# Optimization experiments

Measured on AMD Instinct MI355X. Metric: run time of the kernel, lower is better.

## Reference

```python
import jax, jax.numpy as jnp
import numpy as np


def setup_inputs() -> dict:
    key0 = jax.random.key(0)
    kq, kk, kv, km = jax.random.split(key0, 4)
    B, H, S, Dk = 2, 16, 2048, 64
    query = jax.random.normal(kq, (B, H, S, Dk), dtype=jnp.float32)
    key = jax.random.normal(kk, (B, H, S, Dk), dtype=jnp.float32)
    value = jax.random.normal(kv, (B, H, S, Dk), dtype=jnp.float32)
    mask = jax.random.randint(km, (B, 1, 1, S), 0, 2, dtype=jnp.int32)
    return {"query": query, "key": key, "value": value, "mask": mask}


def reference(query, key, value, mask):
    d_k = query.shape[-1]
    scale = 1.0 / jnp.sqrt(jnp.asarray(d_k, dtype=query.dtype))
    # scores: [B, H, Sq, Sk]
    scores = jnp.einsum("bhqd,bhkd->bhqk", query, key) * scale
    scores = jnp.where(mask == 0, jnp.asarray(-1e9, dtype=scores.dtype), scores)
    attention_weights = jax.nn.softmax(scores, axis=-1)
    output = jnp.einsum("bhqk,bhkd->bhqd", attention_weights, value)
    return output, attention_weights
```

## Files before the change

### kernel.cpp

```cpp
#include <hip/hip_runtime.h>
#include <stdint.h>

#define S_LEN 2048
#define DK 64
#define MT 64
#define NT 64
#define LDP 72

typedef __attribute__((ext_vector_type(8))) short bf16x8;
typedef __attribute__((ext_vector_type(4))) float floatx4;

__device__ inline unsigned short f2bf(float f) {
    union { float f; unsigned u; } v; v.f = f;
    unsigned r = v.u + 0x7FFFu + ((v.u >> 16) & 1u);
    return (unsigned short)(r >> 16);
}

__device__ inline void async16(const void* g, void* l) {
    using gu32 = const __attribute__((address_space(1))) unsigned int;
    using lu32 = __attribute__((address_space(3))) unsigned int;
    gu32* gp = reinterpret_cast<gu32*>(reinterpret_cast<uintptr_t>(g));
    lu32* lp = reinterpret_cast<lu32*>(static_cast<unsigned int>(reinterpret_cast<uintptr_t>(l)));
    __builtin_amdgcn_global_load_lds(gp, lp, 16, 0, 0);
}

__global__ __launch_bounds__(256) void convert_qk(
    const float* __restrict__ Q, const float* __restrict__ K,
    unsigned short* __restrict__ Qb, unsigned short* __restrict__ Kb)
{
    int i = blockIdx.x * 256 + threadIdx.x;
    const int NQ = (2 * 16 * 2048 * 64) / 4;
    const float* src; unsigned short* dst; int j; float sc;
    if (i < NQ) { src = Q; dst = Qb; j = i; sc = 0.125f; }
    else        { src = K; dst = Kb; j = i - NQ; sc = 1.0f; }
    float4 f = ((const float4*)src)[j];
    ushort4 o;
    o.x = f2bf(f.x * sc); o.y = f2bf(f.y * sc);
    o.z = f2bf(f.z * sc); o.w = f2bf(f.w * sc);
    ((ushort4*)dst)[j] = o;
}

__global__ __launch_bounds__(256) void transpose_v(
    const float* __restrict__ V, unsigned short* __restrict__ Vt)
{
    __shared__ unsigned short t[64][72];
    const int head = blockIdx.y, kt = blockIdx.x, tid = threadIdx.x;
    const float* src = V + ((size_t)head * S_LEN + kt * 64) * DK;
    {
        const int r = tid >> 2, c = (tid & 3) * 16;
        #pragma unroll
        for (int i = 0; i < 4; ++i) {
            float4 f = *(const float4*)(src + r * DK + c + i * 4);
            t[r][c + i * 4 + 0] = f2bf(f.x);
            t[r][c + i * 4 + 1] = f2bf(f.y);
            t[r][c + i * 4 + 2] = f2bf(f.z);
            t[r][c + i * 4 + 3] = f2bf(f.w);
        }
    }
    __syncthreads();
    {
        const int d = tid >> 2, kb = (tid & 3) * 16;
        unsigned short tmp[16];
        #pragma unroll
        for (int j = 0; j < 16; ++j) tmp[j] = t[kb + j][d];
        unsigned short* dst = Vt + (size_t)head * DK * S_LEN + (size_t)d * S_LEN + kt * 64 + kb;
        ((uint4*)dst)[0] = *(const uint4*)&tmp[0];
        ((uint4*)dst)[1] = *(const uint4*)&tmp[8];
    }
}

__global__ __launch_bounds__(256) void sdpa_main(
    const unsigned short* __restrict__ Qb, const unsigned short* __restrict__ Kb,
    const unsigned short* __restrict__ Vt, const int* __restrict__ mask,
    float* __restrict__ O, float* __restrict__ W)
{
    __shared__ alignas(16) unsigned short qs[MT * DK];
    __shared__ alignas(16) unsigned short ks[NT * DK];
    __shared__ alignas(16) unsigned short vs[DK * NT];
    __shared__ alignas(16) unsigned short ps[MT * LDP];

    const int tid  = threadIdx.x;
    const int wave = tid >> 6;
    const int lane = tid & 63;
    const int quad = lane >> 4;
    const int l16  = lane & 15;

    const int head = blockIdx.y;
    const int bidx = head >> 4;
    const int q0   = blockIdx.x * MT;

    const unsigned short* Qh = Qb + ((size_t)head * S_LEN + q0) * DK;
    const unsigned short* Kh = Kb + (size_t)head * S_LEN * DK;
    const unsigned short* Vh = Vt + (size_t)head * DK * S_LEN;
    const int*   mk = mask + bidx * S_LEN;
    float* Wh = W + (size_t)head * S_LEN * S_LEN;
    float* Oh = O + (size_t)head * S_LEN * DK;

    {
        const int o0 = wave * 2048 + lane * 16;
        async16((const char*)Qh + o0,        (char*)qs + o0);
        async16((const char*)Qh + o0 + 1024, (char*)qs + o0 + 1024);
    }
    __syncthreads();
    const bf16x8 qa0 = *(const bf16x8*)&qs[(wave * 16 + l16) * DK + quad * 8];
    const bf16x8 qa1 = *(const bf16x8*)&qs[(wave * 16 + l16) * DK + 32 + quad * 8];

    float lsum[4] = {0.f, 0.f, 0.f, 0.f};
    for (int kt = 0; kt < S_LEN / NT; ++kt) {
        {
            const char* gb = (const char*)Kh + kt * 8192;
            const int o0 = wave * 2048 + lane * 16;
            async16(gb + o0,        (char*)ks + o0);
            async16(gb + o0 + 1024, (char*)ks + o0 + 1024);
        }
        float mf[4];
        #pragma unroll
        for (int c = 0; c < 4; ++c)
            mf[c] = mk[kt * NT + c * 16 + l16] ? 1.0f : 0.0f;
        __syncthreads();
        #pragma unroll
        for (int c = 0; c < 4; ++c) {
            bf16x8 b0 = *(const bf16x8*)&ks[(c * 16 + l16) * DK + quad * 8];
            bf16x8 b1 = *(const bf16x8*)&ks[(c * 16 + l16) * DK + 32 + quad * 8];
            floatx4 z = {0.f, 0.f, 0.f, 0.f};
            z = __builtin_amdgcn_mfma_f32_16x16x32_bf16(qa0, b0, z, 0, 0, 0);
            z = __builtin_amdgcn_mfma_f32_16x16x32_bf16(qa1, b1, z, 0, 0, 0);
            #pragma unroll
            for (int r = 0; r < 4; ++r)
                lsum[r] += __expf(z[r]) * mf[c];
        }
        __syncthreads();
    }
    float rl[4];
    #pragma unroll
    for (int r = 0; r < 4; ++r) {
        float s = lsum[r];
        #pragma unroll
        for (int off = 1; off < 16; off <<= 1)
            s += __shfl_xor(s, off, 64);
        rl[r] = 1.0f / s;
    }

    floatx4 oacc[4];
    #pragma unroll
    for (int c = 0; c < 4; ++c) oacc[c] = (floatx4){0.f, 0.f, 0.f, 0.f};

    for (int kt = 0; kt < S_LEN / NT; ++kt) {
        {
            const char* gb = (const char*)Kh + kt * 8192;
            const int o0 = wave * 2048 + lane * 16;
            async16(gb + o0,        (char*)ks + o0);
            async16(gb + o0 + 1024, (char*)ks + o0 + 1024);
        }
        {
            const int o0 = wave * 2048 + lane * 16;
            #pragma unroll
            for (int j = 0; j < 2; ++j) {
                const int o = o0 + j * 1024;
                const int d = o >> 7;
                const int kb = o & 127;
                async16((const char*)Vh + (size_t)d * 4096 + kt * 128 + kb, (char*)vs + o);
            }
        }
        float mf[4];
        #pragma unroll
        for (int c = 0; c < 4; ++c)
            mf[c] = mk[kt * NT + c * 16 + l16] ? 1.0f : 0.0f;
        __syncthreads();

        floatx4 acc[4];
        #pragma unroll
        for (int c = 0; c < 4; ++c) {
            bf16x8 b0 = *(const bf16x8*)&ks[(c * 16 + l16) * DK + quad * 8];
            bf16x8 b1 = *(const bf16x8*)&ks[(c * 16 + l16) * DK + 32 + quad * 8];
            floatx4 z = {0.f, 0.f, 0.f, 0.f};
            z = __builtin_amdgcn_mfma_f32_16x16x32_bf16(qa0, b0, z, 0, 0, 0);
            z = __builtin_amdgcn_mfma_f32_16x16x32_bf16(qa1, b1, z, 0, 0, 0);
            acc[c] = z;
        }

        #pragma unroll
        for (int c = 0; c < 4; ++c) {
            #pragma unroll
            for (int r = 0; r < 4; ++r) {
                const int lrow = wave * 16 + quad * 4 + r;
                float w = __expf(acc[c][r]) * rl[r] * mf[c];
                Wh[(size_t)(q0 + lrow) * S_LEN + kt * NT + c * 16 + l16] = w;
                ps[lrow * LDP + c * 16 + l16] = f2bf(w);
            }
        }
        bf16x8 pa0 = *(const bf16x8*)&ps[(wave * 16 + l16) * LDP + quad * 8];
        bf16x8 pa1 = *(const bf16x8*)&ps[(wave * 16 + l16) * LDP + 32 + quad * 8];
        #pragma unroll
        for (int c = 0; c < 4; ++c) {
            bf16x8 v0 = *(const bf16x8*)&vs[(c * 16 + l16) * DK + quad * 8];
            bf16x8 v1 = *(const bf16x8*)&vs[(c * 16 + l16) * DK + 32 + quad * 8];
            oacc[c] = __builtin_amdgcn_mfma_f32_16x16x32_bf16(pa0, v0, oacc[c], 0, 0, 0);
            oacc[c] = __builtin_amdgcn_mfma_f32_16x16x32_bf16(pa1, v1, oacc[c], 0, 0, 0);
        }
        __syncthreads();
    }

    #pragma unroll
    for (int c = 0; c < 4; ++c) {
        #pragma unroll
        for (int r = 0; r < 4; ++r) {
            const int lrow = wave * 16 + quad * 4 + r;
            Oh[(size_t)(q0 + lrow) * DK + c * 16 + l16] = oacc[c][r];
        }
    }
}

#define LD 72
__global__ __launch_bounds__(256) void sdpa_fb(
    const float* __restrict__ Q, const float* __restrict__ K,
    const float* __restrict__ V, const int* __restrict__ mask,
    float* __restrict__ O, float* __restrict__ W)
{
    __shared__ alignas(16) unsigned short qs[MT * LD];
    __shared__ alignas(16) unsigned short ks[NT * LD];
    __shared__ alignas(16) unsigned short vs[DK * LD];
    __shared__ alignas(16) unsigned short ps[MT * LD];
    __shared__ float addm[NT];

    const int tid = threadIdx.x, wave = tid >> 6, lane = tid & 63;
    const int quad = lane >> 4, l16 = lane & 15;
    const int head = blockIdx.y, bidx = head >> 4, q0 = blockIdx.x * MT;

    const float* Qh = Q + (size_t)head * S_LEN * DK;
    const float* Kh = K + (size_t)head * S_LEN * DK;
    const float* Vh = V + (size_t)head * S_LEN * DK;
    const int* mk = mask + bidx * S_LEN;
    float* Wh = W + (size_t)head * S_LEN * S_LEN;
    float* Oh = O + (size_t)head * S_LEN * DK;

    #pragma unroll
    for (int i = 0; i < 4; ++i) {
        const int g = i * 256 + tid, row = g >> 4, col = (g & 15) * 4;
        float4 f = *(const float4*)(Qh + (size_t)(q0 + row) * DK + col);
        unsigned* d = (unsigned*)&qs[row * LD + col];
        d[0] = f2bf(f.x) | ((unsigned)f2bf(f.y) << 16);
        d[1] = f2bf(f.z) | ((unsigned)f2bf(f.w) << 16);
    }
    __syncthreads();
    const bf16x8 qa0 = *(const bf16x8*)&qs[(wave * 16 + l16) * LD + quad * 8];
    const bf16x8 qa1 = *(const bf16x8*)&qs[(wave * 16 + l16) * LD + 32 + quad * 8];

    float m[4], l[4];
    #pragma unroll
    for (int r = 0; r < 4; ++r) { m[r] = -1e30f; l[r] = 0.0f; }

    for (int kt = 0; kt < S_LEN / NT; ++kt) {
        #pragma unroll
        for (int i = 0; i < 4; ++i) {
            const int g = i * 256 + tid, row = g >> 4, col = (g & 15) * 4;
            float4 f = *(const float4*)(Kh + (size_t)(kt * NT + row) * DK + col);
            unsigned* d = (unsigned*)&ks[row * LD + col];
            d[0] = f2bf(f.x) | ((unsigned)f2bf(f.y) << 16);
            d[1] = f2bf(f.z) | ((unsigned)f2bf(f.w) << 16);
        }
        if (tid < NT) addm[tid] = mk[kt * NT + tid] ? 0.0f : -1e30f;
        __syncthreads();
        floatx4 acc[4];
        #pragma unroll
        for (int c = 0; c < 4; ++c) {
            bf16x8 b0 = *(const bf16x8*)&ks[(c * 16 + l16) * LD + quad * 8];
            bf16x8 b1 = *(const bf16x8*)&ks[(c * 16 + l16) * LD + 32 + quad * 8];
            floatx4 z = {0.f, 0.f, 0.f, 0.f};
            z = __builtin_amdgcn_mfma_f32_16x16x32_bf16(qa0, b0, z, 0, 0, 0);
            z = __builtin_amdgcn_mfma_f32_16x16x32_bf16(qa1, b1, z, 0, 0, 0);
            acc[c] = z;
        }
        float sv[4][4];
        #pragma unroll
        for (int c = 0; c < 4; ++c) {
            float am = addm[c * 16 + l16];
            #pragma unroll
            for (int r = 0; r < 4; ++r) sv[c][r] = acc[c][r] * 0.125f + am;
        }
        #pragma unroll
        for (int r = 0; r < 4; ++r) {
            float tmax = fmaxf(fmaxf(sv[0][r], sv[1][r]), fmaxf(sv[2][r], sv[3][r]));
            #pragma unroll
            for (int off = 1; off < 16; off <<= 1) tmax = fmaxf(tmax, __shfl_xor(tmax, off, 64));
            float mn = fmaxf(m[r], tmax);
            float ts = __expf(sv[0][r] - mn) + __expf(sv[1][r] - mn)
                     + __expf(sv[2][r] - mn) + __expf(sv[3][r] - mn);
            #pragma unroll
            for (int off = 1; off < 16; off <<= 1) ts += __shfl_xor(ts, off, 64);
            l[r] = l[r] * __expf(m[r] - mn) + ts;
            m[r] = mn;
        }
        __syncthreads();
    }
    float rl[4];
    #pragma unroll
    for (int r = 0; r < 4; ++r) rl[r] = 1.0f / l[r];

    floatx4 oacc[4];
    #pragma unroll
    for (int c = 0; c < 4; ++c) oacc[c] = (floatx4){0.f, 0.f, 0.f, 0.f};

    for (int kt = 0; kt < S_LEN / NT; ++kt) {
        #pragma unroll
        for (int i = 0; i < 4; ++i) {
            const int g = i * 256 + tid, row = g >> 4, col = (g & 15) * 4;
            float4 f = *(const float4*)(Kh + (size_t)(kt * NT + row) * DK + col);
            unsigned* d = (unsigned*)&ks[row * LD + col];
            d[0] = f2bf(f.x) | ((unsigned)f2bf(f.y) << 16);
            d[1] = f2bf(f.z) | ((unsigned)f2bf(f.w) << 16);
        }
        {
            const int row = tid >> 2, colg = (tid & 3) << 4;
            const float4* vsrc = (const float4*)(Vh + (size_t)(kt * NT + row) * DK + colg);
            #pragma unroll
            for (int i = 0; i < 4; ++i) {
                float4 f = vsrc[i];
                const int dbase = colg + i * 4;
                vs[(dbase + 0) * LD + row] = f2bf(f.x);
                vs[(dbase + 1) * LD + row] = f2bf(f.y);
                vs[(dbase + 2) * LD + row] = f2bf(f.z);
                vs[(dbase + 3) * LD + row] = f2bf(f.w);
            }
        }
        if (tid < NT) addm[tid] = mk[kt * NT + tid] ? 0.0f : -1e30f;
        __syncthreads();
        floatx4 acc[4];
        #pragma unroll
        for (int c = 0; c < 4; ++c) {
            bf16x8 b0 = *(const bf16x8*)&ks[(c * 16 + l16) * LD + quad * 8];
            bf16x8 b1 = *(const bf16x8*)&ks[(c * 16 + l16) * LD + 32 + quad * 8];
            floatx4 z = {0.f, 0.f, 0.f, 0.f};
            z = __builtin_amdgcn_mfma_f32_16x16x32_bf16(qa0, b0, z, 0, 0, 0);
            z = __builtin_amdgcn_mfma_f32_16x16x32_bf16(qa1, b1, z, 0, 0, 0);
            acc[c] = z;
        }
        #pragma unroll
        for (int c = 0; c < 4; ++c) {
            float am = addm[c * 16 + l16];
            #pragma unroll
            for (int r = 0; r < 4; ++r) {
                const int lrow = wave * 16 + quad * 4 + r;
                float w = __expf(acc[c][r] * 0.125f + am - m[r]) * rl[r];
                Wh[(size_t)(q0 + lrow) * S_LEN + kt * NT + c * 16 + l16] = w;
                ps[lrow * LD + c * 16 + l16] = f2bf(w);
            }
        }
        __syncthreads();
        bf16x8 pa0 = *(const bf16x8*)&ps[(wave * 16 + l16) * LD + quad * 8];
        bf16x8 pa1 = *(const bf16x8*)&ps[(wave * 16 + l16) * LD + 32 + quad * 8];
        #pragma unroll
        for (int c = 0; c < 4; ++c) {
            bf16x8 v0 = *(const bf16x8*)&vs[(c * 16 + l16) * LD + quad * 8];
            bf16x8 v1 = *(const bf16x8*)&vs[(c * 16 + l16) * LD + 32 + quad * 8];
            oacc[c] = __builtin_amdgcn_mfma_f32_16x16x32_bf16(pa0, v0, oacc[c], 0, 0, 0);
            oacc[c] = __builtin_amdgcn_mfma_f32_16x16x32_bf16(pa1, v1, oacc[c], 0, 0, 0);
        }
        __syncthreads();
    }
    #pragma unroll
    for (int c = 0; c < 4; ++c) {
        #pragma unroll
        for (int r = 0; r < 4; ++r) {
            const int lrow = wave * 16 + quad * 4 + r;
            Oh[(size_t)(q0 + lrow) * DK + c * 16 + l16] = oacc[c][r];
        }
    }
}

extern "C" void kernel_launch(void* const* d_in, const int* in_sizes, int n_in,
                              void* d_out, int out_size, void* d_ws, size_t ws_size,
                              hipStream_t stream) {
    const float* Q  = (const float*)d_in[0];
    const float* K  = (const float*)d_in[1];
    const float* V  = (const float*)d_in[2];
    const int* mask = (const int*)d_in[3];

    float* O = (float*)d_out;
    float* W = (float*)d_out + (size_t)2 * 16 * 2048 * 64;

    const size_t elems = (size_t)2 * 16 * 2048 * 64;
    const size_t need  = 3 * elems * sizeof(unsigned short);

    if (ws_size >= need) {
        unsigned short* Qb = (unsigned short*)d_ws;
        unsigned short* Kb = Qb + elems;
        unsigned short* Vt = Kb + elems;
        convert_qk<<<dim3((2 * elems / 4) / 256), 256, 0, stream>>>(Q, K, Qb, Kb);
        transpose_v<<<dim3(32, 32), 256, 0, stream>>>(V, Vt);
        sdpa_main<<<dim3(S_LEN / MT, 32), 256, 0, stream>>>(Qb, Kb, Vt, mask, O, W);
    } else {
        sdpa_fb<<<dim3(S_LEN / MT, 32), 256, 0, stream>>>(Q, K, V, mask, O, W);
    }
}
```

Baseline: 683.3 us.

## Rewrite sdpa_main with 32x32 MFMA, swizzled LDS, double-buffered K/V staging

Switches the main attention kernel from 16x16x32 to 32x32x16 bf16 MFMAs. Each wave now owns a 32-query by 32-key subtile and the two key-halves are reduced through LDS at the end. K and V tiles are double-buffered, so the next tile's async load overlaps current compute, and an XOR swizzle on LDS offsets avoids bank conflicts. The mask is read once as a ballot bitmask, W is written as float4 instead of scalars, and the P tile reaches the second MFMA through permlane32_swap rather than an LDS round trip. The costs are more register pressure from 16-wide accumulators, an extra cross-wave reduction for lsum and O, and more intricate index math that could hide layout bugs.

```diff
diff --git a/kernel.cpp b/kernel.cpp
--- a/kernel.cpp
+++ b/kernel.cpp
@@ -5,10 +5,12 @@
 #define DK 64
 #define MT 64
 #define NT 64
-#define LDP 72
+#define LD 72
 
 typedef __attribute__((ext_vector_type(8))) short bf16x8;
 typedef __attribute__((ext_vector_type(4))) float floatx4;
+typedef __attribute__((ext_vector_type(16))) float f32x16;
+typedef __attribute__((ext_vector_type(2))) unsigned int uint2v;
 
 __device__ inline unsigned short f2bf(float f) {
     union { float f; unsigned u; } v; v.f = f;
@@ -22,6 +24,24 @@
     gu32* gp = reinterpret_cast<gu32*>(reinterpret_cast<uintptr_t>(g));
     lu32* lp = reinterpret_cast<lu32*>(static_cast<unsigned int>(reinterpret_cast<uintptr_t>(l)));
     __builtin_amdgcn_global_load_lds(gp, lp, 16, 0, 0);
+}
+
+__device__ inline unsigned swz(unsigned o) { return o ^ ((o >> 3) & 0x70u); }
+
+__device__ inline void stage8k(const char* g, char* l, int wave, int lane) {
+    const unsigned o0 = (unsigned)(wave * 2048 + lane * 16);
+    async16(g + swz(o0), l + o0);
+    async16(g + swz(o0 + 1024), l + o0 + 1024);
+}
+
+__device__ inline void stageV(const char* Vh, int kt, char* l, int wave, int lane) {
+    const unsigned o0 = (unsigned)(wave * 2048 + lane * 16);
+    #pragma unroll
+    for (int j = 0; j < 2; ++j) {
+        const unsigned o = o0 + j * 1024;
+        const unsigned s = swz(o);
+        async16(Vh + (size_t)(o >> 7) * 4096 + kt * 128 + (s & 127), l + o);
+    }
 }
 
 __global__ __launch_bounds__(256) void convert_qk(
@@ -74,144 +94,152 @@
     const unsigned short* __restrict__ Vt, const int* __restrict__ mask,
     float* __restrict__ O, float* __restrict__ W)
 {
-    __shared__ alignas(16) unsigned short qs[MT * DK];
-    __shared__ alignas(16) unsigned short ks[NT * DK];
-    __shared__ alignas(16) unsigned short vs[DK * NT];
-    __shared__ alignas(16) unsigned short ps[MT * LDP];
+    __shared__ alignas(16) char lds[32768];
+    __shared__ float red[4][32];
 
     const int tid  = threadIdx.x;
     const int wave = tid >> 6;
     const int lane = tid & 63;
-    const int quad = lane >> 4;
-    const int l16  = lane & 15;
+    const int l31  = lane & 31;
+    const int hi   = lane >> 5;
+    const int qg   = wave >> 1;
+    const int kb   = wave & 1;
 
     const int head = blockIdx.y;
     const int bidx = head >> 4;
     const int q0   = blockIdx.x * MT;
 
-    const unsigned short* Qh = Qb + ((size_t)head * S_LEN + q0) * DK;
-    const unsigned short* Kh = Kb + (size_t)head * S_LEN * DK;
-    const unsigned short* Vh = Vt + (size_t)head * DK * S_LEN;
-    const int*   mk = mask + bidx * S_LEN;
+    const char* Qh = (const char*)(Qb + ((size_t)head * S_LEN + q0) * DK);
+    const char* Kh = (const char*)(Kb + (size_t)head * S_LEN * DK);
+    const char* Vh = (const char*)(Vt + (size_t)head * DK * S_LEN);
+    const int*  mk = mask + bidx * S_LEN;
     float* Wh = W + (size_t)head * S_LEN * S_LEN;
     float* Oh = O + (size_t)head * S_LEN * DK;
 
+    char* B0 = lds;
+    char* B1 = lds + 8192;
+    char* B2 = lds + 16384;
+    char* B3 = lds + 24576;
+
+    stage8k(Qh, B0, wave, lane);
+    stage8k(Kh, B1, wave, lane);
+    __syncthreads();
+
+    bf16x8 qf[4];
     {
-        const int o0 = wave * 2048 + lane * 16;
-        async16((const char*)Qh + o0,        (char*)qs + o0);
-        async16((const char*)Qh + o0 + 1024, (char*)qs + o0 + 1024);
-    }
-    __syncthreads();
-    const bf16x8 qa0 = *(const bf16x8*)&qs[(wave * 16 + l16) * DK + quad * 8];
-    const bf16x8 qa1 = *(const bf16x8*)&qs[(wave * 16 + l16) * DK + 32 + quad * 8];
-
-    float lsum[4] = {0.f, 0.f, 0.f, 0.f};
-    for (int kt = 0; kt < S_LEN / NT; ++kt) {
+        const unsigned rq = (unsigned)(qg * 32 + l31) * 128;
+        #pragma unroll
+        for (int m = 0; m < 4; ++m)
+            qf[m] = *(const bf16x8*)(B0 + swz(rq + m * 32 + hi * 16));
+    }
+
+    const unsigned rk = (unsigned)(kb * 32 + l31) * 128;
+
+    float lsum = 0.f;
+    for (int t = 0; t < 32; ++t) {
+        char* cur = (t & 1) ? B2 : B1;
+        if (t < 31) stage8k(Kh + (size_t)(t + 1) * 8192, (t & 1) ? B1 : B2, wave, lane);
+        const unsigned long long mm = __ballot(mk[t * 64 + lane] != 0);
+        const unsigned mw = (unsigned)(mm >> (kb * 32));
+        f32x16 z;
+        #pragma unroll
+        for (int r = 0; r < 16; ++r) z[r] = 0.f;
+        #pragma unroll
+        for (int m = 0; m < 4; ++m) {
+            bf16x8 kf = *(const bf16x8*)(cur + swz(rk + m * 32 + hi * 16));
+            z = __builtin_amdgcn_mfma_f32_32x32x16_bf16(kf, qf[m], z, 0, 0, 0);
+        }
+        #pragma unroll
+        for (int r = 0; r < 16; ++r) {
+            const int kl = (r & 3) + 8 * (r >> 2) + 4 * hi;
+            lsum += ((mw >> kl) & 1u) ? __expf(z[r]) : 0.f;
+        }
+        __syncthreads();
+    }
+    lsum += __shfl_xor(lsum, 32);
+    if (hi == 0) red[wave][l31] = lsum;
+    __syncthreads();
+    const float rl = 1.0f / (red[qg * 2][l31] + red[qg * 2 + 1][l31]);
+
+    f32x16 oacc0, oacc1;
+    #pragma unroll
+    for (int r = 0; r < 16; ++r) { oacc0[r] = 0.f; oacc1[r] = 0.f; }
+
+    stage8k(Kh, B0, wave, lane);
+    stageV(Vh, 0, B2, wave, lane);
+    __syncthreads();
+
+    for (int t = 0; t < 32; ++t) {
+        char* curK = (t & 1) ? B1 : B0;
+        char* curV = (t & 1) ? B3 : B2;
+        if (t < 31) {
+            stage8k(Kh + (size_t)(t + 1) * 8192, (t & 1) ? B0 : B1, wave, lane);
+            stageV(Vh, t + 1, (t & 1) ? B2 : B3, wave, lane);
+        }
+        const unsigned long long mm = __ballot(mk[t * 64 + lane] != 0);
+        const unsigned mw = (unsigned)(mm >> (kb * 32));
+
+        f32x16 z;
+        #pragma unroll
+        for (int r = 0; r < 16; ++r) z[r] = 0.f;
+        #pragma unroll
+        for (int m = 0; m < 4; ++m) {
+            bf16x8 kf = *(const bf16x8*)(curK + swz(rk + m * 32 + hi * 16));
+            z = __builtin_amdgcn_mfma_f32_32x32x16_bf16(kf, qf[m], z, 0, 0, 0);
+        }
+        #pragma unroll
+        for (int r = 0; r < 16; ++r) {
+            const int kl = (r & 3) + 8 * (r >> 2) + 4 * hi;
+            const float e = __expf(z[r]) * rl;
+            z[r] = ((mw >> kl) & 1u) ? e : 0.f;
+        }
         {
-            const char* gb = (const char*)Kh + kt * 8192;
-            const int o0 = wave * 2048 + lane * 16;
-            async16(gb + o0,        (char*)ks + o0);
-            async16(gb + o0 + 1024, (char*)ks + o0 + 1024);
-        }
-        float mf[4];
-        #pragma unroll
-        for (int c = 0; c < 4; ++c)
-            mf[c] = mk[kt * NT + c * 16 + l16] ? 1.0f : 0.0f;
-        __syncthreads();
-        #pragma unroll
-        for (int c = 0; c < 4; ++c) {
-            bf16x8 b0 = *(const bf16x8*)&ks[(c * 16 + l16) * DK + quad * 8];
-            bf16x8 b1 = *(const bf16x8*)&ks[(c * 16 + l16) * DK + 32 + quad * 8];
-            floatx4 z = {0.f, 0.f, 0.f, 0.f};
-            z = __builtin_amdgcn_mfma_f32_16x16x32_bf16(qa0, b0, z, 0, 0, 0);
-            z = __builtin_amdgcn_mfma_f32_16x16x32_bf16(qa1, b1, z, 0, 0, 0);
-            #pragma unroll
-            for (int r = 0; r < 4; ++r)
-                lsum[r] += __expf(z[r]) * mf[c];
-        }
-        __syncthreads();
-    }
-    float rl[4];
-    #pragma unroll
-    for (int r = 0; r < 4; ++r) {
-        float s = lsum[r];
-        #pragma unroll
-        for (int off = 1; off < 16; off <<= 1)
-            s += __shfl_xor(s, off, 64);
-        rl[r] = 1.0f / s;
-    }
-
-    floatx4 oacc[4];
-    #pragma unroll
-    for (int c = 0; c < 4; ++c) oacc[c] = (floatx4){0.f, 0.f, 0.f, 0.f};
-
-    for (int kt = 0; kt < S_LEN / NT; ++kt) {
-        {
-            const char* gb = (const char*)Kh + kt * 8192;
-            const int o0 = wave * 2048 + lane * 16;
-            async16(gb + o0,        (char*)ks + o0);
-            async16(gb + o0 + 1024, (char*)ks + o0 + 1024);
-        }
-        {
-            const int o0 = wave * 2048 + lane * 16;
-            #pragma unroll
-            for (int j = 0; j < 2; ++j) {
-                const int o = o0 + j * 1024;
-                const int d = o >> 7;
-                const int kb = o & 127;
-                async16((const char*)Vh + (size_t)d * 4096 + kt * 128 + kb, (char*)vs + o);
-            }
-        }
-        float mf[4];
-        #pragma unroll
-        for (int c = 0; c < 4; ++c)
-            mf[c] = mk[kt * NT + c * 16 + l16] ? 1.0f : 0.0f;
-        __syncthreads();
-
-        floatx4 acc[4];
-        #pragma unroll
-        for (int c = 0; c < 4; ++c) {
-            bf16x8 b0 = *(const bf16x8*)&ks[(c * 16 + l16) * DK + quad * 8];
-            bf16x8 b1 = *(const bf16x8*)&ks[(c * 16 + l16) * DK + 32 + quad * 8];
-            floatx4 z = {0.f, 0.f, 0.f, 0.f};
-            z = __builtin_amdgcn_mfma_f32_16x16x32_bf16(qa0, b0, z, 0, 0, 0);
-            z = __builtin_amdgcn_mfma_f32_16x16x32_bf16(qa1, b1, z, 0, 0, 0);
-            acc[c] = z;
-        }
-
-        #pragma unroll
-        for (int c = 0; c < 4; ++c) {
-            #pragma unroll
-            for (int r = 0; r < 4; ++r) {
-                const int lrow = wave * 16 + quad * 4 + r;
-                float w = __expf(acc[c][r]) * rl[r] * mf[c];
-                Wh[(size_t)(q0 + lrow) * S_LEN + kt * NT + c * 16 + l16] = w;
-                ps[lrow * LDP + c * 16 + l16] = f2bf(w);
-            }
-        }
-        bf16x8 pa0 = *(const bf16x8*)&ps[(wave * 16 + l16) * LDP + quad * 8];
-        bf16x8 pa1 = *(const bf16x8*)&ps[(wave * 16 + l16) * LDP + 32 + quad * 8];
-        #pragma unroll
-        for (int c = 0; c < 4; ++c) {
-            bf16x8 v0 = *(const bf16x8*)&vs[(c * 16 + l16) * DK + quad * 8];
-            bf16x8 v1 = *(const bf16x8*)&vs[(c * 16 + l16) * DK + 32 + quad * 8];
-            oacc[c] = __builtin_amdgcn_mfma_f32_16x16x32_bf16(pa0, v0, oacc[c], 0, 0, 0);
-            oacc[c] = __builtin_amdgcn_mfma_f32_16x16x32_bf16(pa1, v1, oacc[c], 0, 0, 0);
-        }
-        __syncthreads();
-    }
-
-    #pragma unroll
-    for (int c = 0; c < 4; ++c) {
-        #pragma unroll
-        for (int r = 0; r < 4; ++r) {
-            const int lrow = wave * 16 + quad * 4 + r;
-            Oh[(size_t)(q0 + lrow) * DK + c * 16 + l16] = oacc[c][r];
-        }
-    }
-}
-
-#define LD 72
+            float* wp = Wh + (size_t)(q0 + qg * 32 + l31) * S_LEN + t * 64 + kb * 32 + 4 * hi;
+            #pragma unroll
+            for (int g = 0; g < 4; ++g)
+                *(float4*)(wp + 8 * g) = make_float4(z[4*g], z[4*g+1], z[4*g+2], z[4*g+3]);
+        }
+        unsigned pk0[4], pk1[4];
+        #pragma unroll
+        for (int g = 0; g < 4; ++g) {
+            pk0[g] = (unsigned)f2bf(z[4*g+0]) | ((unsigned)f2bf(z[4*g+1]) << 16);
+            pk1[g] = (unsigned)f2bf(z[4*g+2]) | ((unsigned)f2bf(z[4*g+3]) << 16);
+        }
+        #pragma unroll
+        for (int m2 = 0; m2 < 2; ++m2) {
+            uint2v s0 = __builtin_amdgcn_permlane32_swap(pk0[2*m2], pk0[2*m2+1], false, false);
+            uint2v s1 = __builtin_amdgcn_permlane32_swap(pk1[2*m2], pk1[2*m2+1], false, false);
+            union { unsigned u[4]; bf16x8 v; } pa;
+            pa.u[0] = s0[0]; pa.u[1] = s1[0]; pa.u[2] = s0[1]; pa.u[3] = s1[1];
+            const unsigned cv = (unsigned)(kb * 64 + m2 * 32 + hi * 16);
+            bf16x8 v0 = *(const bf16x8*)(curV + swz((unsigned)l31 * 128 + cv));
+            bf16x8 v1 = *(const bf16x8*)(curV + swz((unsigned)(32 + l31) * 128 + cv));
+            oacc0 = __builtin_amdgcn_mfma_f32_32x32x16_bf16(v0, pa.v, oacc0, 0, 0, 0);
+            oacc1 = __builtin_amdgcn_mfma_f32_32x32x16_bf16(v1, pa.v, oacc1, 0, 0, 0);
+        }
+        __syncthreads();
+    }
+
+    float* redO = (float*)lds;
+    if (kb == 1) {
+        float* dst = redO + (size_t)(qg * 64 + lane) * 32;
+        #pragma unroll
+        for (int r = 0; r < 16; ++r) { dst[r] = oacc0[r]; dst[16 + r] = oacc1[r]; }
+    }
+    __syncthreads();
+    if (kb == 0) {
+        const float* sp = redO + (size_t)(qg * 64 + lane) * 32;
+        #pragma unroll
+        for (int r = 0; r < 16; ++r) { oacc0[r] += sp[r]; oacc1[r] += sp[16 + r]; }
+        float* op = Oh + (size_t)(q0 + qg * 32 + l31) * DK + 4 * hi;
+        #pragma unroll
+        for (int g = 0; g < 4; ++g) {
+            *(float4*)(op + 8 * g)      = make_float4(oacc0[4*g], oacc0[4*g+1], oacc0[4*g+2], oacc0[4*g+3]);
+            *(float4*)(op + 32 + 8 * g) = make_float4(oacc1[4*g], oacc1[4*g+1], oacc1[4*g+2], oacc1[4*g+3]);
+        }
+    }
+}
+
 __global__ __launch_bounds__(256) void sdpa_fb(
     const float* __restrict__ Q, const float* __restrict__ K,
     const float* __restrict__ V, const int* __restrict__ mask,
```

Result: slower. 716.7 us (+4.9%).
